# Performance work log

Hardware: AMD Instinct MI355X
Metric: run time of the kernel (lower is better)

The kernel has to match this reference:

```python
import jax, jax.numpy as jnp
import numpy as np

N = 20000
E = 320000
IN = 256
H = 4
C = 64
NEG_SLOPE = 0.2


def setup_inputs() -> dict:
    key = jax.random.key(0)
    ks = jax.random.split(key, 12)
    HC = H * C

    def w(k, shape, fan_in):
        return jax.random.normal(k, shape, dtype=jnp.float32) / np.sqrt(fan_in)

    x = jax.random.normal(ks[0], (N, IN), dtype=jnp.float32)
    edge_index = jax.random.randint(ks[1], (2, E), 0, N, dtype=jnp.int64)
    return {
        "x": x,
        "edge_index": edge_index,
        "Wl1": w(ks[2], (IN, HC), IN),
        "Wr1": w(ks[3], (IN, HC), IN),
        "att1": w(ks[4], (H, C), C),
        "b1": jnp.zeros((HC,), dtype=jnp.float32),
        "Wl2": w(ks[5], (HC, HC), HC),
        "Wr2": w(ks[6], (HC, HC), HC),
        "att2": w(ks[7], (H, C), C),
        "b2": jnp.zeros((HC,), dtype=jnp.float32),
        "Wfc": w(ks[8], (HC, 2), HC),
        "bfc": jnp.zeros((2,), dtype=jnp.float32),
    }


def _gatv2(x, src, dst, Wl, Wr, att, b):
    """GATv2Conv (concat=True, share_weights=False), inference (no dropout)."""
    n = x.shape[0]
    xl = (x @ Wl).reshape(n, H, C)  # source-side projection
    xr = (x @ Wr).reshape(n, H, C)  # target-side projection
    # per-edge GATv2 score: a^T LeakyReLU(xl_j + xr_i)
    e = jax.nn.leaky_relu(xl[src] + xr[dst], NEG_SLOPE)      # [E, H, C]
    score = jnp.einsum("ehc,hc->eh", e, att)                 # [E, H]
    # segment softmax over incoming edges of each target node
    smax = jax.ops.segment_max(score, dst, num_segments=n)   # [N, H]
    ex = jnp.exp(score - smax[dst])
    denom = jax.ops.segment_sum(ex, dst, num_segments=n)     # [N, H]
    alpha = ex / denom[dst]                                  # [E, H]
    # scatter-aggregate messages (source projections weighted by alpha)
    out = jax.ops.segment_sum(alpha[:, :, None] * xl[src], dst, num_segments=n)
    return out.reshape(n, H * C) + b


def reference(x, edge_index, Wl1, Wr1, att1, b1, Wl2, Wr2, att2, b2, Wfc, bfc):
    n = x.shape[0]
    # add_self_loops=True (PyG default)
    loop = jnp.arange(n, dtype=edge_index.dtype)
    src = jnp.concatenate([edge_index[0], loop])
    dst = jnp.concatenate([edge_index[1], loop])

    h = _gatv2(x, src, dst, Wl1, Wr1, att1, b1)
    h = jax.nn.relu(h)
    h = _gatv2(h, src, dst, Wl2, Wr2, att2, b2)
    h = jax.nn.relu(h)
    g = jnp.mean(h, axis=0, keepdims=True)  # [1, H*C]
    return g @ Wfc + bfc                    # [1, 2]
```

## Files before the change

kernel.cpp:

```cpp
#include <hip/hip_runtime.h>
#include <hip/hip_bf16.h>
#include <math.h>

#define Nn 20000
#define Ee 320000
#define INF_ 256
#define Hh 4
#define Cc 64
#define HC 256
#define NEG_SLOPE 0.2f

using frag16 = __attribute__((ext_vector_type(8))) short;
using f32x4  = __attribute__((ext_vector_type(4))) float;

__device__ __forceinline__ void async16(const void* g, void* l) {
    __builtin_amdgcn_global_load_lds(
        (const __attribute__((address_space(1))) unsigned int*)g,
        (__attribute__((address_space(3))) unsigned int*)l,
        16, 0, 0);
}


__global__ void init_deg(int* deg, int n) {
    int i = blockIdx.x * blockDim.x + threadIdx.x;
    if (i < n) deg[i] = 1;
}

__global__ void hist_kernel(const int* __restrict__ dst, int ne, int* deg) {
    int e = blockIdx.x * blockDim.x + threadIdx.x;
    if (e < ne) atomicAdd(&deg[dst[e]], 1);
}

__global__ __launch_bounds__(256) void scan1(const int* __restrict__ deg,
                                             int* __restrict__ excl,
                                             int* __restrict__ bsum, int n) {
    int tid = threadIdx.x;
    int gid = blockIdx.x * 256 + tid;
    int lane = tid & 63;
    int v = (gid < n) ? deg[gid] : 0;
    int x = v;
    #pragma unroll
    for (int off = 1; off < 64; off <<= 1) {
        int y = __shfl_up(x, off, 64);
        if (lane >= off) x += y;
    }
    __shared__ int wsum[4];
    if (lane == 63) wsum[tid >> 6] = x;
    __syncthreads();
    int wadd = 0;
    for (int w = 0; w < (tid >> 6); ++w) wadd += wsum[w];
    int incl = x + wadd;
    if (gid < n) excl[gid] = incl - v;
    if (tid == 255) bsum[blockIdx.x] = incl;
}

__global__ void scan2(const int* __restrict__ bsum, int* __restrict__ boff, int nb) {
    int lane = threadIdx.x;
    int carry = 0;
    for (int base = 0; base < nb; base += 64) {
        int i = base + lane;
        int v = (i < nb) ? bsum[i] : 0;
        int x = v;
        #pragma unroll
        for (int off = 1; off < 64; off <<= 1) {
            int y = __shfl_up(x, off, 64);
            if (lane >= off) x += y;
        }
        if (i < nb) boff[i] = carry + x - v;
        carry += __shfl(x, 63, 64);
    }
    if (lane == 0) boff[nb] = carry;
}

__global__ void scan_add(int* __restrict__ row_start, int* __restrict__ cursor,
                         const int* __restrict__ boff, int n, int nb) {
    int gid = blockIdx.x * blockDim.x + threadIdx.x;
    if (gid < n) {
        int v = row_start[gid] + boff[gid >> 8];
        row_start[gid] = v;
        cursor[gid] = v;
    }
    if (gid == n) row_start[n] = boff[nb];
}

__global__ void scatter_kernel(const int* __restrict__ src, const int* __restrict__ dst,
                               int ne, int n, int* cursor, int* colx) {
    int e = blockIdx.x * blockDim.x + threadIdx.x;
    if (e < ne) {
        int d = dst[e];
        int pos = atomicAdd(&cursor[d], 1);
        colx[pos] = src[e];
    } else if (e < ne + n) {
        int node = e - ne;
        int pos = atomicAdd(&cursor[node], 1);
        colx[pos] = node;
    }
}


__device__ inline unsigned short bf16rn(float f) {
    unsigned u = __float_as_uint(f);
    unsigned r = (u + 0x7FFFu + ((u >> 16) & 1u)) >> 16;
    return (unsigned short)r;
}

__device__ inline void split1(float v, short& h, short& l) {
    unsigned short hh = bf16rn(v);
    float back = __uint_as_float(((unsigned)hh) << 16);
    unsigned short ll = bf16rn(v - back);
    h = (short)hh; l = (short)ll;
}

__device__ __forceinline__ float4 bf4_to_f4(ushort4 u) {
    return make_float4(__uint_as_float((unsigned)u.x << 16),
                       __uint_as_float((unsigned)u.y << 16),
                       __uint_as_float((unsigned)u.z << 16),
                       __uint_as_float((unsigned)u.w << 16));
}

__global__ __launch_bounds__(256) void split_kernel(const float* __restrict__ in,
                                                    short* __restrict__ hi,
                                                    short* __restrict__ lo, int n4) {
    int i = blockIdx.x * blockDim.x + threadIdx.x;
    if (i >= n4) return;
    float4 v = ((const float4*)in)[i];
    short4 h, l;
    split1(v.x, h.x, l.x);
    split1(v.y, h.y, l.y);
    split1(v.z, h.z, l.z);
    split1(v.w, h.w, l.w);
    ((short4*)hi)[i] = h;
    ((short4*)lo)[i] = l;
}

__global__ __launch_bounds__(256) void wsplit_all(const float* __restrict__ Wl1,
                                                  const float* __restrict__ Wr1,
                                                  const float* __restrict__ Wl2,
                                                  const float* __restrict__ Wr2,
                                                  short* __restrict__ WhT1,
                                                  short* __restrict__ WlT1,
                                                  short* __restrict__ WhT2,
                                                  short* __restrict__ WlT2) {
    int b = blockIdx.x;
    int n = b & 255;
    int k = threadIdx.x;
    const float* W = (b < 256) ? Wl1 : (b < 512) ? Wr1 : (b < 768) ? Wl2 : Wr2;
    short* Wh = (b < 512) ? WhT1 : WhT2;
    short* Wl = (b < 512) ? WlT1 : WlT2;
    int col = b & 511;
    float v = W[k * 256 + n];
    short h, l;
    split1(v, h, l);
    Wh[col * 256 + k] = h;
    Wl[col * 256 + k] = l;
}


#define BK 32

__global__ __launch_bounds__(256) void mfma_gemm(const short* __restrict__ Ah,
                                                 const short* __restrict__ Al,
                                                 const short* __restrict__ WhT,
                                                 const short* __restrict__ WlT,
                                                 unsigned short* __restrict__ XLh,
                                                 float* __restrict__ XR) {
    __shared__ short As_h[128 * BK];
    __shared__ short As_l[128 * BK];
    __shared__ short Bs_h[128 * BK];
    __shared__ short Bs_l[128 * BK];
    int tid = threadIdx.x;
    int wave = tid >> 6, lane = tid & 63;
    int quad = lane >> 4, lc = lane & 15;
    int bx = blockIdx.x;
    int bm = blockIdx.y * 128;
    int cbase = (bx * 128) & 255;

    int sr0 = wave * 32 + (lane >> 2);
    int sr1 = sr0 + 16;
    int koff = (lane & 3) * 8;
    int ga0 = bm + sr0; if (ga0 >= Nn) ga0 = Nn - 1;
    int ga1 = bm + sr1; if (ga1 >= Nn) ga1 = Nn - 1;
    int gb0 = bx * 128 + sr0;
    int gb1 = bx * 128 + sr1;
    int j0 = wave * 2, j1 = j0 + 1;

    f32x4 acc[2][8] = {};
    for (int c = 0; c < 8; ++c) {
        int k0 = c * BK;
        async16(Ah  + (size_t)ga0 * HC + k0 + koff, &As_h[j0 * 512]);
        async16(Ah  + (size_t)ga1 * HC + k0 + koff, &As_h[j1 * 512]);
        async16(Al  + (size_t)ga0 * HC + k0 + koff, &As_l[j0 * 512]);
        async16(Al  + (size_t)ga1 * HC + k0 + koff, &As_l[j1 * 512]);
        async16(WhT + (size_t)gb0 * HC + k0 + koff, &Bs_h[j0 * 512]);
        async16(WhT + (size_t)gb1 * HC + k0 + koff, &Bs_h[j1 * 512]);
        async16(WlT + (size_t)gb0 * HC + k0 + koff, &Bs_l[j0 * 512]);
        async16(WlT + (size_t)gb1 * HC + k0 + koff, &Bs_l[j1 * 512]);
        __syncthreads();

        frag16 a0h = *(const frag16*)&As_h[(wave * 32 + lc) * BK + quad * 8];
        frag16 a1h = *(const frag16*)&As_h[(wave * 32 + 16 + lc) * BK + quad * 8];
        frag16 a0l = *(const frag16*)&As_l[(wave * 32 + lc) * BK + quad * 8];
        frag16 a1l = *(const frag16*)&As_l[(wave * 32 + 16 + lc) * BK + quad * 8];
        #pragma unroll
        for (int t = 0; t < 8; ++t) {
            frag16 bh = *(const frag16*)&Bs_h[(t * 16 + lc) * BK + quad * 8];
            frag16 bl = *(const frag16*)&Bs_l[(t * 16 + lc) * BK + quad * 8];
            acc[0][t] = __builtin_amdgcn_mfma_f32_16x16x32_bf16(a0h, bh, acc[0][t], 0, 0, 0);
            acc[1][t] = __builtin_amdgcn_mfma_f32_16x16x32_bf16(a1h, bh, acc[1][t], 0, 0, 0);
            acc[0][t] = __builtin_amdgcn_mfma_f32_16x16x32_bf16(a0l, bh, acc[0][t], 0, 0, 0);
            acc[1][t] = __builtin_amdgcn_mfma_f32_16x16x32_bf16(a1l, bh, acc[1][t], 0, 0, 0);
            acc[0][t] = __builtin_amdgcn_mfma_f32_16x16x32_bf16(a0h, bl, acc[0][t], 0, 0, 0);
            acc[1][t] = __builtin_amdgcn_mfma_f32_16x16x32_bf16(a1h, bl, acc[1][t], 0, 0, 0);
        }
        __syncthreads();
    }
    #pragma unroll
    for (int mt = 0; mt < 2; ++mt) {
        int rbase = bm + wave * 32 + mt * 16 + quad * 4;
        #pragma unroll
        for (int t = 0; t < 8; ++t) {
            int col = cbase + t * 16 + lc;
            #pragma unroll
            for (int r = 0; r < 4; ++r) {
                int rw = rbase + r;
                if (rw >= Nn) continue;
                if (bx < 2) XLh[(size_t)rw * HC + col] = bf16rn(acc[mt][t][r]);
                else        XR [(size_t)rw * HC + col] = acc[mt][t][r];
            }
        }
    }
}


__device__ __forceinline__ float edge_score(const float4 v, const float4 xr,
                                            const float4 a06, const float4 a04) {
    float tx = v.x + xr.x, ty = v.y + xr.y, tz = v.z + xr.z, tw = v.w + xr.w;
    float p = a06.x * tx + a04.x * fabsf(tx);
    p += a06.y * ty + a04.y * fabsf(ty);
    p += a06.z * tz + a04.z * fabsf(tz);
    p += a06.w * tw + a04.w * fabsf(tw);
    p += __shfl_xor(p, 1, 64);
    p += __shfl_xor(p, 2, 64);
    p += __shfl_xor(p, 4, 64);
    p += __shfl_xor(p, 8, 64);
    return p;
}

__global__ __launch_bounds__(256) void gat_kernel(const ushort4* __restrict__ XL4,
                                                  const float4* __restrict__ XR4,
                                                  const int* __restrict__ row_start,
                                                  const int* __restrict__ colx,
                                                  const float4* __restrict__ att4,
                                                  const float4* __restrict__ bias4,
                                                  float4* __restrict__ Hout,
                                                  short4* __restrict__ Ahi,
                                                  short4* __restrict__ Alo,
                                                  int mode) {
    int wave = threadIdx.x >> 6, lane = threadIdx.x & 63;
    int node = blockIdx.x * 4 + wave;
    float4 xr = XR4[(size_t)node * 64 + lane];
    float4 a  = att4[lane];
    float4 a06 = make_float4(a.x * 0.6f, a.y * 0.6f, a.z * 0.6f, a.w * 0.6f);
    float4 a04 = make_float4(a.x * 0.4f, a.y * 0.4f, a.z * 0.4f, a.w * 0.4f);
    int e0 = row_start[node], e1 = row_start[node + 1];
    float l0 = 0.f, l1 = 0.f;
    float4 acc0 = make_float4(0.f, 0.f, 0.f, 0.f);
    float4 acc1 = make_float4(0.f, 0.f, 0.f, 0.f);
    int e = e0;
    for (; e + 1 < e1; e += 2) {
        int s0 = __builtin_amdgcn_readfirstlane(colx[e]);
        int s1 = __builtin_amdgcn_readfirstlane(colx[e + 1]);
        ushort4 u0 = XL4[(size_t)s0 * 64 + lane];
        ushort4 u1 = XL4[(size_t)s1 * 64 + lane];
        float4 v0 = bf4_to_f4(u0);
        float4 v1 = bf4_to_f4(u1);
        float pe0 = __expf(edge_score(v0, xr, a06, a04));
        float pe1 = __expf(edge_score(v1, xr, a06, a04));
        l0 += pe0; l1 += pe1;
        acc0.x += pe0 * v0.x; acc0.y += pe0 * v0.y;
        acc0.z += pe0 * v0.z; acc0.w += pe0 * v0.w;
        acc1.x += pe1 * v1.x; acc1.y += pe1 * v1.y;
        acc1.z += pe1 * v1.z; acc1.w += pe1 * v1.w;
    }
    if (e < e1) {
        int s0 = __builtin_amdgcn_readfirstlane(colx[e]);
        float4 v0 = bf4_to_f4(XL4[(size_t)s0 * 64 + lane]);
        float pe0 = __expf(edge_score(v0, xr, a06, a04));
        l0 += pe0;
        acc0.x += pe0 * v0.x; acc0.y += pe0 * v0.y;
        acc0.z += pe0 * v0.z; acc0.w += pe0 * v0.w;
    }
    float rl = 1.f / (l0 + l1);
    float4 b = bias4[lane];
    float4 o = make_float4(fmaxf((acc0.x + acc1.x) * rl + b.x, 0.f),
                           fmaxf((acc0.y + acc1.y) * rl + b.y, 0.f),
                           fmaxf((acc0.z + acc1.z) * rl + b.z, 0.f),
                           fmaxf((acc0.w + acc1.w) * rl + b.w, 0.f));
    size_t oidx = (size_t)node * 64 + lane;
    if (mode) {
        short4 h4, l4;
        split1(o.x, h4.x, l4.x);
        split1(o.y, h4.y, l4.y);
        split1(o.z, h4.z, l4.z);
        split1(o.w, h4.w, l4.w);
        Ahi[oidx] = h4;
        Alo[oidx] = l4;
    } else {
        Hout[oidx] = o;
    }
}


__global__ void zero_f(float* p, int n) {
    int i = blockIdx.x * blockDim.x + threadIdx.x;
    if (i < n) p[i] = 0.f;
}

__global__ __launch_bounds__(256) void colsum_kernel(const float* __restrict__ Hmat,
                                                     float* __restrict__ g, int n) {
    int ch = threadIdx.x;
    float s = 0.f;
    for (int r = blockIdx.x; r < n; r += gridDim.x)
        s += Hmat[(size_t)r * HC + ch];
    atomicAdd(&g[ch], s);
}

__global__ __launch_bounds__(256) void fc_kernel(const float* __restrict__ g,
                                                 const float* __restrict__ Wfc,
                                                 const float* __restrict__ bfc,
                                                 float* __restrict__ out, float invN) {
    int t = threadIdx.x;
    float gv = g[t] * invN;
    float p0 = gv * Wfc[2 * t];
    float p1 = gv * Wfc[2 * t + 1];
    #pragma unroll
    for (int off = 32; off > 0; off >>= 1) {
        p0 += __shfl_xor(p0, off, 64);
        p1 += __shfl_xor(p1, off, 64);
    }
    __shared__ float s0[4], s1[4];
    if ((t & 63) == 0) { s0[t >> 6] = p0; s1[t >> 6] = p1; }
    __syncthreads();
    if (t == 0) {
        out[0] = s0[0] + s0[1] + s0[2] + s0[3] + bfc[0];
        out[1] = s1[0] + s1[1] + s1[2] + s1[3] + bfc[1];
    }
}


extern "C" void kernel_launch(void* const* d_in, const int* in_sizes, int n_in,
                              void* d_out, int out_size, void* d_ws, size_t ws_size,
                              hipStream_t stream) {
    const float* x    = (const float*)d_in[0];
    const int*   eidx = (const int*)d_in[1];
    const float* Wl1  = (const float*)d_in[2];
    const float* Wr1  = (const float*)d_in[3];
    const float* att1 = (const float*)d_in[4];
    const float* b1   = (const float*)d_in[5];
    const float* Wl2  = (const float*)d_in[6];
    const float* Wr2  = (const float*)d_in[7];
    const float* att2 = (const float*)d_in[8];
    const float* b2   = (const float*)d_in[9];
    const float* Wfc  = (const float*)d_in[10];
    const float* bfc  = (const float*)d_in[11];
    float* out = (float*)d_out;

    const int* srcv = eidx;
    const int* dstv = eidx + Ee;

    size_t NHC = (size_t)Nn * HC;
    float* XR = (float*)d_ws;
    float* Hb = XR + NHC;
    float* g  = Hb + NHC;
    unsigned short* XLh = (unsigned short*)(g + HC);
    short* Ah   = (short*)(XLh + NHC);
    short* Al   = Ah + NHC;
    short* WhT1 = Al + NHC;
    short* WlT1 = WhT1 + 512 * 256;
    short* WhT2 = WlT1 + 512 * 256;
    short* WlT2 = WhT2 + 512 * 256;
    int* deg       = (int*)(WlT2 + 512 * 256);
    int* row_start = deg + Nn;
    int* cursor    = row_start + (Nn + 1);
    int* colx      = cursor + Nn;
    int* bsum      = colx + (Ee + Nn);
    int* boff      = bsum + 128;

    const int NB = (Nn + 255) / 256;
    const int N4 = (int)(NHC / 4);

    init_deg<<<(Nn + 255) / 256, 256, 0, stream>>>(deg, Nn);
    hist_kernel<<<(Ee + 255) / 256, 256, 0, stream>>>(dstv, Ee, deg);
    scan1<<<NB, 256, 0, stream>>>(deg, row_start, bsum, Nn);
    scan2<<<1, 64, 0, stream>>>(bsum, boff, NB);
    scan_add<<<(Nn + 256) / 256, 256, 0, stream>>>(row_start, cursor, boff, Nn, NB);
    scatter_kernel<<<(Ee + Nn + 255) / 256, 256, 0, stream>>>(srcv, dstv, Ee, Nn, cursor, colx);

    dim3 ggrid(4, (Nn + 127) / 128);

    wsplit_all<<<1024, 256, 0, stream>>>(Wl1, Wr1, Wl2, Wr2, WhT1, WlT1, WhT2, WlT2);
    split_kernel<<<(N4 + 255) / 256, 256, 0, stream>>>(x, Ah, Al, N4);

    mfma_gemm<<<ggrid, 256, 0, stream>>>(Ah, Al, WhT1, WlT1, XLh, XR);
    gat_kernel<<<Nn / 4, 256, 0, stream>>>((const ushort4*)XLh, (const float4*)XR,
                                           row_start, colx, (const float4*)att1,
                                           (const float4*)b1, (float4*)Hb,
                                           (short4*)Ah, (short4*)Al, 1);

    mfma_gemm<<<ggrid, 256, 0, stream>>>(Ah, Al, WhT2, WlT2, XLh, XR);
    gat_kernel<<<Nn / 4, 256, 0, stream>>>((const ushort4*)XLh, (const float4*)XR,
                                           row_start, colx, (const float4*)att2,
                                           (const float4*)b2, (float4*)Hb,
                                           (short4*)Ah, (short4*)Al, 0);

    zero_f<<<1, 256, 0, stream>>>(g, HC);
    colsum_kernel<<<256, 256, 0, stream>>>(Hb, g, Nn);
    fc_kernel<<<1, 256, 0, stream>>>(g, Wfc, bfc, out, 1.0f / Nn);
}
```

Before: 294.6 us.

## Load GEMM fragments directly from global memory instead of staging through LDS

Result: slower. 395.8 us (+34.3%).

```diff
diff --git a/kernel.cpp b/kernel.cpp
--- a/kernel.cpp
+++ b/kernel.cpp
@@ -12,13 +12,6 @@
 
 using frag16 = __attribute__((ext_vector_type(8))) short;
 using f32x4  = __attribute__((ext_vector_type(4))) float;
-
-__device__ __forceinline__ void async16(const void* g, void* l) {
-    __builtin_amdgcn_global_load_lds(
-        (const __attribute__((address_space(1))) unsigned int*)g,
-        (__attribute__((address_space(3))) unsigned int*)l,
-        16, 0, 0);
-}
 
 
 __global__ void init_deg(int* deg, int n) {
@@ -156,55 +149,42 @@
 }
 
 
-#define BK 32
-
 __global__ __launch_bounds__(256) void mfma_gemm(const short* __restrict__ Ah,
                                                  const short* __restrict__ Al,
                                                  const short* __restrict__ WhT,
                                                  const short* __restrict__ WlT,
                                                  unsigned short* __restrict__ XLh,
                                                  float* __restrict__ XR) {
-    __shared__ short As_h[128 * BK];
-    __shared__ short As_l[128 * BK];
-    __shared__ short Bs_h[128 * BK];
-    __shared__ short Bs_l[128 * BK];
     int tid = threadIdx.x;
     int wave = tid >> 6, lane = tid & 63;
     int quad = lane >> 4, lc = lane & 15;
-    int bx = blockIdx.x;
-    int bm = blockIdx.y * 128;
+    int bx = blockIdx.y;
+    int bm = blockIdx.x * 128;
     int cbase = (bx * 128) & 255;
 
-    int sr0 = wave * 32 + (lane >> 2);
-    int sr1 = sr0 + 16;
-    int koff = (lane & 3) * 8;
-    int ga0 = bm + sr0; if (ga0 >= Nn) ga0 = Nn - 1;
-    int ga1 = bm + sr1; if (ga1 >= Nn) ga1 = Nn - 1;
-    int gb0 = bx * 128 + sr0;
-    int gb1 = bx * 128 + sr1;
-    int j0 = wave * 2, j1 = j0 + 1;
+    int row0 = bm + wave * 32 + lc;
+    int row1 = row0 + 16;
+    int ca0 = (row0 < Nn) ? row0 : (Nn - 1);
+    int ca1 = (row1 < Nn) ? row1 : (Nn - 1);
+
+    const short* pa0h = Ah  + (size_t)ca0 * HC + quad * 8;
+    const short* pa1h = Ah  + (size_t)ca1 * HC + quad * 8;
+    const short* pa0l = Al  + (size_t)ca0 * HC + quad * 8;
+    const short* pa1l = Al  + (size_t)ca1 * HC + quad * 8;
+    const short* pbh  = WhT + (size_t)(bx * 128 + lc) * HC + quad * 8;
+    const short* pbl  = WlT + (size_t)(bx * 128 + lc) * HC + quad * 8;
 
     f32x4 acc[2][8] = {};
     for (int c = 0; c < 8; ++c) {
-        int k0 = c * BK;
-        async16(Ah  + (size_t)ga0 * HC + k0 + koff, &As_h[j0 * 512]);
-        async16(Ah  + (size_t)ga1 * HC + k0 + koff, &As_h[j1 * 512]);
-        async16(Al  + (size_t)ga0 * HC + k0 + koff, &As_l[j0 * 512]);
-        async16(Al  + (size_t)ga1 * HC + k0 + koff, &As_l[j1 * 512]);
-        async16(WhT + (size_t)gb0 * HC + k0 + koff, &Bs_h[j0 * 512]);
-        async16(WhT + (size_t)gb1 * HC + k0 + koff, &Bs_h[j1 * 512]);
-        async16(WlT + (size_t)gb0 * HC + k0 + koff, &Bs_l[j0 * 512]);
-        async16(WlT + (size_t)gb1 * HC + k0 + koff, &Bs_l[j1 * 512]);
-        __syncthreads();
-
-        frag16 a0h = *(const frag16*)&As_h[(wave * 32 + lc) * BK + quad * 8];
-        frag16 a1h = *(const frag16*)&As_h[(wave * 32 + 16 + lc) * BK + quad * 8];
-        frag16 a0l = *(const frag16*)&As_l[(wave * 32 + lc) * BK + quad * 8];
-        frag16 a1l = *(const frag16*)&As_l[(wave * 32 + 16 + lc) * BK + quad * 8];
+        int k0 = c * 32;
+        frag16 a0h = *(const frag16*)(pa0h + k0);
+        frag16 a1h = *(const frag16*)(pa1h + k0);
+        frag16 a0l = *(const frag16*)(pa0l + k0);
+        frag16 a1l = *(const frag16*)(pa1l + k0);
         #pragma unroll
         for (int t = 0; t < 8; ++t) {
-            frag16 bh = *(const frag16*)&Bs_h[(t * 16 + lc) * BK + quad * 8];
-            frag16 bl = *(const frag16*)&Bs_l[(t * 16 + lc) * BK + quad * 8];
+            frag16 bh = *(const frag16*)(pbh + (size_t)t * 16 * HC + k0);
+            frag16 bl = *(const frag16*)(pbl + (size_t)t * 16 * HC + k0);
             acc[0][t] = __builtin_amdgcn_mfma_f32_16x16x32_bf16(a0h, bh, acc[0][t], 0, 0, 0);
             acc[1][t] = __builtin_amdgcn_mfma_f32_16x16x32_bf16(a1h, bh, acc[1][t], 0, 0, 0);
             acc[0][t] = __builtin_amdgcn_mfma_f32_16x16x32_bf16(a0l, bh, acc[0][t], 0, 0, 0);
@@ -212,7 +192,6 @@
             acc[0][t] = __builtin_amdgcn_mfma_f32_16x16x32_bf16(a0h, bl, acc[0][t], 0, 0, 0);
             acc[1][t] = __builtin_amdgcn_mfma_f32_16x16x32_bf16(a1h, bl, acc[1][t], 0, 0, 0);
         }
-        __syncthreads();
     }
     #pragma unroll
     for (int mt = 0; mt < 2; ++mt) {
@@ -396,7 +375,7 @@
     scan_add<<<(Nn + 256) / 256, 256, 0, stream>>>(row_start, cursor, boff, Nn, NB);
     scatter_kernel<<<(Ee + Nn + 255) / 256, 256, 0, stream>>>(srcv, dstv, Ee, Nn, cursor, colx);
 
-    dim3 ggrid(4, (Nn + 127) / 128);
+    dim3 ggrid((Nn + 127) / 128, 4);
 
     wsplit_all<<<1024, 256, 0, stream>>>(Wl1, Wr1, Wl2, Wr2, WhT1, WlT1, WhT2, WlT2);
     split_kernel<<<(N4 + 255) / 256, 256, 0, stream>>>(x, Ah, Al, N4);
```
